# Kernel optimization log

Measured on AMD Instinct MI355X. Metric: run time of the kernel, lower is better.

Reference implementation:

```python
import jax, jax.numpy as jnp
import numpy as np

B, P, T = 64, 196, 30
E, D, A, ENC, V = 512, 512, 512, 512, 30000


def setup_inputs() -> dict:
    key = jax.random.key(0)
    ks = jax.random.split(key, 24)
    s = 0.02
    return {
        "encoder_feats": jax.random.normal(ks[0], (B, P, ENC), jnp.float32),
        "encoder_pooled": jax.random.normal(ks[1], (B, ENC), jnp.float32),
        "captions": jax.random.randint(ks[2], (B, T), 0, V),
        "We_att": jax.random.normal(ks[3], (ENC, A), jnp.float32) * s,
        "be_att": jnp.zeros((A,), jnp.float32),
        "Wd_att": jax.random.normal(ks[4], (D, A), jnp.float32) * s,
        "bd_att": jnp.zeros((A,), jnp.float32),
        "wf_att": jax.random.normal(ks[5], (A, 1), jnp.float32) * s,
        "bf_att": jnp.zeros((), jnp.float32),
        "emb_table": jax.random.normal(ks[6], (V, E), jnp.float32) * s,
        "W_ih": jax.random.normal(ks[7], (E + ENC, 4 * D), jnp.float32) * s,
        "W_hh": jax.random.normal(ks[8], (D, 4 * D), jnp.float32) * s,
        "b_ih": jnp.zeros((4 * D,), jnp.float32),
        "b_hh": jnp.zeros((4 * D,), jnp.float32),
        "W_init_h": jax.random.normal(ks[9], (ENC, D), jnp.float32) * s,
        "b_init_h": jnp.zeros((D,), jnp.float32),
        "W_init_c": jax.random.normal(ks[10], (ENC, D), jnp.float32) * s,
        "b_init_c": jnp.zeros((D,), jnp.float32),
        "W_fc": jax.random.normal(ks[11], (D, V), jnp.float32) * s,
        "b_fc": jnp.zeros((V,), jnp.float32),
        "W_beta": jax.random.normal(ks[12], (D, ENC), jnp.float32) * s,
        "b_beta": jnp.zeros((ENC,), jnp.float32),
    }


def reference(encoder_feats, encoder_pooled, captions, We_att, be_att, Wd_att,
              bd_att, wf_att, bf_att, emb_table, W_ih, W_hh, b_ih, b_hh,
              W_init_h, b_init_h, W_init_c, b_init_c, W_fc, b_fc, W_beta, b_beta):
    # teacher_forcing_ratio = 1.0, dropout in eval mode (identity)
    emb = emb_table[captions]                              # (B, T, E)
    h = jnp.tanh(encoder_pooled @ W_init_h + b_init_h)     # (B, D)
    c = jnp.tanh(encoder_pooled @ W_init_c + b_init_c)
    enc_proj = encoder_feats @ We_att + be_att             # (B, P, A) precomputed

    def step(carry, emb_t):
        h, c = carry
        dec_proj = h @ Wd_att + bd_att                     # (B, A)
        e = jnp.tanh(enc_proj + dec_proj[:, None, :])      # (B, P, A)
        scores = jnp.squeeze(e @ wf_att, -1) + bf_att      # (B, P)
        alpha = jax.nn.softmax(scores, axis=1)
        ctx = jnp.einsum('bp,bpd->bd', alpha, encoder_feats)
        gate = jax.nn.sigmoid(h @ W_beta + b_beta)
        ctx = gate * ctx
        x = jnp.concatenate([emb_t, ctx], axis=1)          # (B, E+ENC)
        gates = x @ W_ih + b_ih + h @ W_hh + b_hh          # (B, 4D) torch order i,f,g,o
        i, f, g, o = jnp.split(gates, 4, axis=1)
        c2 = jax.nn.sigmoid(f) * c + jax.nn.sigmoid(i) * jnp.tanh(g)
        h2 = jax.nn.sigmoid(o) * jnp.tanh(c2)
        out = h2 @ W_fc + b_fc                             # (B, V)
        return (h2, c2), out

    # inputs at steps t=1..T-1 are teacher-forced embeddings[:, t-1]
    xs = jnp.swapaxes(emb[:, :-1, :], 0, 1)                # (T-1, B, E)
    _, outs = jax.lax.scan(step, (h, c), xs)               # (T-1, B, V)
    outs = jnp.swapaxes(outs, 0, 1)                        # (B, T-1, V)
    zero0 = jnp.zeros((outs.shape[0], 1, outs.shape[2]), outs.dtype)
    return jnp.concatenate([zero0, outs], axis=1)          # (B, T, V)
```

## Files before the change

kernel.cpp:

```cpp
#include <hip/hip_runtime.h>
#include <hip/hip_bf16.h>

#define BB 64
#define PP 196
#define TT 30
#define DD 512
#define VV 30000
#define VPAD 30080
#define MROWS 1856
#define MPAD 1920
#define NBLK 64
#define ASTR 3072
#define ABUF ((size_t)64 * ASTR)

typedef __attribute__((ext_vector_type(8))) short short8;
typedef __attribute__((ext_vector_type(4))) float f32x4;

__device__ __forceinline__ unsigned short f2bf(float f) {
    unsigned int u = __float_as_uint(f);
    unsigned int r = u + 0x7FFFu + ((u >> 16) & 1u);
    return (unsigned short)(r >> 16);
}
__device__ __forceinline__ float bf2f(unsigned short u) {
    return __uint_as_float(((unsigned int)u) << 16);
}
__device__ __forceinline__ float sigf(float x) { return 1.f / (1.f + __expf(-x)); }
__device__ __forceinline__ float tanh_fast(float x) { return 1.f - 2.f / (1.f + __expf(2.f * x)); }
__device__ __forceinline__ unsigned int pack2(unsigned short a, unsigned short b) {
    return (unsigned int)a | ((unsigned int)b << 16);
}
__device__ __forceinline__ void ast_u32(unsigned int* p, unsigned int v) {
    __hip_atomic_store(p, v, __ATOMIC_RELAXED, __HIP_MEMORY_SCOPE_AGENT);
}
__device__ __forceinline__ void ast_f32(float* p, float v) {
    __hip_atomic_store(p, v, __ATOMIC_RELAXED, __HIP_MEMORY_SCOPE_AGENT);
}

__global__ __launch_bounds__(256) void k_cast(const float* __restrict__ in,
                                              unsigned short* __restrict__ out, int n) {
    int i = blockIdx.x * 256 + threadIdx.x;
    int stride = gridDim.x * 256;
    for (; i < n; i += stride) out[i] = f2bf(in[i]);
}

__global__ __launch_bounds__(256) void k_transpose_cast(const float* __restrict__ in,
                                                        unsigned short* __restrict__ out,
                                                        int R, int C, int Cpad, int ostride, int ooff) {
    __shared__ float tile[32][33];
    int tx = threadIdx.x & 31, ty = threadIdx.x >> 5;
    int c0 = blockIdx.x * 32, r0 = blockIdx.y * 32;
#pragma unroll
    for (int i = 0; i < 4; ++i) {
        int r = r0 + ty + i * 8, c = c0 + tx;
        tile[ty + i * 8][tx] = (c < C) ? in[(size_t)r * C + c] : 0.f;
    }
    __syncthreads();
#pragma unroll
    for (int i = 0; i < 4; ++i) {
        int outr = c0 + ty + i * 8, outc = r0 + tx;
        if (outr < Cpad) out[(size_t)outr * ostride + ooff + outc] = f2bf(tile[tx][ty + i * 8]);
    }
}

__global__ __launch_bounds__(256) void k_transpose_cast_split(const float* __restrict__ in,
                                                              unsigned short* __restrict__ out,
                                                              int R, int C, int ostride,
                                                              int ooff, int looff) {
    __shared__ float tile[32][33];
    int tx = threadIdx.x & 31, ty = threadIdx.x >> 5;
    int c0 = blockIdx.x * 32, r0 = blockIdx.y * 32;
#pragma unroll
    for (int i = 0; i < 4; ++i) {
        int r = r0 + ty + i * 8, c = c0 + tx;
        tile[ty + i * 8][tx] = in[(size_t)r * C + c];
    }
    __syncthreads();
#pragma unroll
    for (int i = 0; i < 4; ++i) {
        int outr = c0 + ty + i * 8, outc = r0 + tx;
        float v = tile[tx][ty + i * 8];
        unsigned short hi = f2bf(v);
        unsigned short lo = f2bf(v - bf2f(hi));
        out[(size_t)outr * ostride + ooff + outc] = hi;
        out[(size_t)outr * ostride + looff + outc] = lo;
    }
}

__global__ __launch_bounds__(256) void k_zero0(float* __restrict__ out) {
    int i = blockIdx.x * 256 + threadIdx.x;
    int b = i / VV, v = i - b * VV;
    out[(size_t)b * (TT * VV) + v] = 0.f;
}

__global__ __launch_bounds__(256) void k_init(const float* __restrict__ pooled,
                                              const float* __restrict__ Wh, const float* __restrict__ bh,
                                              const float* __restrict__ Wc, const float* __restrict__ bc,
                                              unsigned short* __restrict__ A1,
                                              float* __restrict__ cbuf, int* __restrict__ bar) {
    int b = blockIdx.x >> 1, which = blockIdx.x & 1, t = threadIdx.x;
    if (blockIdx.x == 0) {
        for (int i = t; i < NBLK * 32 + 32; i += 256) bar[i] = 0;
    }
    const float* W = which ? Wc : Wh;
    const float* bias = which ? bc : bh;
    const float* pr = pooled + b * DD;
    float a0 = 0.f, a1 = 0.f;
#pragma unroll 4
    for (int k = 0; k < DD; ++k) {
        float pv = pr[k];
        a0 += pv * W[k * DD + t];
        a1 += pv * W[k * DD + t + 256];
    }
    float v0 = tanh_fast(a0 + bias[t]);
    float v1 = tanh_fast(a1 + bias[t + 256]);
    if (which == 0) {
        unsigned short hi0 = f2bf(v0), lo0 = f2bf(v0 - bf2f(hi0));
        unsigned short hi1 = f2bf(v1), lo1 = f2bf(v1 - bf2f(hi1));
        unsigned short* xr = A1 + b * ASTR;
        xr[1024 + t] = hi0;        xr[2560 + t] = lo0;
        xr[1024 + t + 256] = hi1;  xr[2560 + t + 256] = lo1;
    } else {
        cbuf[b * DD + t] = v0;
        cbuf[b * DD + t + 256] = v1;
    }
}

__device__ __forceinline__ void gbar(int* bar, int g) {
    __syncthreads();
    asm volatile("s_waitcnt vmcnt(0)" ::: "memory");
    if (blockIdx.x == 0) {
        int t = threadIdx.x;
        if (t >= 1 && t < NBLK) {
            while (__hip_atomic_load(&bar[t * 32], __ATOMIC_RELAXED, __HIP_MEMORY_SCOPE_AGENT) < g)
                __builtin_amdgcn_s_sleep(1);
        }
        __syncthreads();
        if (t == 0)
            __hip_atomic_store(&bar[NBLK * 32], g, __ATOMIC_RELAXED, __HIP_MEMORY_SCOPE_AGENT);
    } else {
        if (threadIdx.x == 0) {
            __hip_atomic_store(&bar[blockIdx.x * 32], g, __ATOMIC_RELAXED, __HIP_MEMORY_SCOPE_AGENT);
            while (__hip_atomic_load(&bar[NBLK * 32], __ATOMIC_RELAXED, __HIP_MEMORY_SCOPE_AGENT) < g)
                __builtin_amdgcn_s_sleep(1);
        }
        __syncthreads();
    }
}

__global__ __launch_bounds__(256, 1) void k_recur(
    const unsigned short* __restrict__ ep,
    const unsigned short* __restrict__ fb,
    const unsigned short* __restrict__ WdbT,
    const unsigned short* __restrict__ WT,
    const float* __restrict__ bd,
    const float* __restrict__ bbeta,
    const float* __restrict__ wfv,
    const int* __restrict__ caps,
    const float* __restrict__ emb,
    const float* __restrict__ b_ih,
    const float* __restrict__ b_hh,
    unsigned short* __restrict__ A_rot,
    float* __restrict__ cbuf,
    float* __restrict__ dpb_rot,
    unsigned short* __restrict__ hb,
    int* __restrict__ bar) {

    const int blk = blockIdx.x, t = threadIdx.x;
    const int lane = t & 63, wave = t >> 6;
    const int r16 = lane & 15, kg = lane >> 4;
    const int swz = kg ^ ((r16 >> 1) & 3);

    __shared__ unsigned short Bp_s[16 * 1024];
    __shared__ unsigned short Sa[2][2048];
    __shared__ unsigned short Sl[2][2048];
    __shared__ unsigned short Sb[2][2048];
    __shared__ unsigned short Sbl[2][2048];
    __shared__ float sc_s[256];
    __shared__ float red_s[16];
    __shared__ float ctx_s[4][512];

    const int srow = t >> 2, scs = t & 3;
    const int scsrc = scs ^ ((srow >> 1) & 3);

    {
        const unsigned short* src = WdbT + (size_t)(blk * 16) * 1024;
#pragma unroll
        for (int cc = 0; cc < 8; ++cc) {
            int c = t + cc * 256;
            int row = c >> 7, u = c & 127;
            ((uint4*)Bp_s)[row * 128 + (u ^ (row & 7))] =
                *(const uint4*)(src + (size_t)row * 1024 + u * 8);
        }
    }
    __syncthreads();

    int gph = 0;

    for (int ts = 1; ts < TT; ++ts) {
        unsigned short* Acur = A_rot + (size_t)ts * ABUF;
        unsigned short* Anext = Acur + ABUF;
        float* dpb = dpb_rot + (size_t)(ts - 1) * 64 * 1024;

        {
            const int n0 = blk * 16;
            const unsigned short* Ah = Acur + srow * ASTR + 1024 + scsrc * 8;
            const unsigned short* Al = Acur + srow * ASTR + 2560 + scsrc * 8;
            f32x4 acc = {0.f, 0.f, 0.f, 0.f};
            uint4 p0h = *(const uint4*)(Ah + 0), p0l = *(const uint4*)(Al + 0);
            uint4 p1h = *(const uint4*)(Ah + 32), p1l = *(const uint4*)(Al + 32);
#pragma unroll 1
            for (int i = 0; i < 16; i += 2) {
                ((uint4*)Sa[0])[t] = p0h;
                ((uint4*)Sl[0])[t] = p0l;
                { int kn = (i + 2 < 16 ? i + 2 : i) * 32;
                  p0h = *(const uint4*)(Ah + kn); p0l = *(const uint4*)(Al + kn); }
                __syncthreads();
                {
                    int k0 = i * 32;
                    short8 ah = *(const short8*)&Sa[0][((wave * 16 + r16) * 4 + swz) * 8];
                    short8 al = *(const short8*)&Sl[0][((wave * 16 + r16) * 4 + swz) * 8];
                    int cu = (k0 >> 3) + kg;
                    short8 bh = *(const short8*)&Bp_s[r16 * 1024 + ((cu ^ (r16 & 7)) << 3)];
                    short8 bl = *(const short8*)&Bp_s[r16 * 1024 + (((cu + 64) ^ (r16 & 7)) << 3)];
                    acc = __builtin_amdgcn_mfma_f32_16x16x32_bf16(ah, bh, acc, 0, 0, 0);
                    acc = __builtin_amdgcn_mfma_f32_16x16x32_bf16(al, bh, acc, 0, 0, 0);
                    acc = __builtin_amdgcn_mfma_f32_16x16x32_bf16(ah, bl, acc, 0, 0, 0);
                }
                ((uint4*)Sa[1])[t] = p1h;
                ((uint4*)Sl[1])[t] = p1l;
                { int kn = (i + 3 < 16 ? i + 3 : i + 1) * 32;
                  p1h = *(const uint4*)(Ah + kn); p1l = *(const uint4*)(Al + kn); }
                __syncthreads();
                {
                    int k0 = (i + 1) * 32;
                    short8 ah = *(const short8*)&Sa[1][((wave * 16 + r16) * 4 + swz) * 8];
                    short8 al = *(const short8*)&Sl[1][((wave * 16 + r16) * 4 + swz) * 8];
                    int cu = (k0 >> 3) + kg;
                    short8 bh = *(const short8*)&Bp_s[r16 * 1024 + ((cu ^ (r16 & 7)) << 3)];
                    short8 bl = *(const short8*)&Bp_s[r16 * 1024 + (((cu + 64) ^ (r16 & 7)) << 3)];
                    acc = __builtin_amdgcn_mfma_f32_16x16x32_bf16(ah, bh, acc, 0, 0, 0);
                    acc = __builtin_amdgcn_mfma_f32_16x16x32_bf16(al, bh, acc, 0, 0, 0);
                    acc = __builtin_amdgcn_mfma_f32_16x16x32_bf16(ah, bl, acc, 0, 0, 0);
                }
            }
            int col = n0 + r16;
#pragma unroll
            for (int r = 0; r < 4; ++r) {
                int b = wave * 16 + kg * 4 + r;
                float v = acc[r];
                if (col < 512) ast_f32(&dpb[b * 1024 + col], v + bd[col]);
                else ast_f32(&dpb[b * 1024 + col], sigf(v + bbeta[col - 512]));
            }
        }
        gbar(bar, ++gph);

        {
            const int b = blk;
            const int d8 = lane * 8;
            float dsl[8], wsl[8];
            {
                float4 dv0 = *(const float4*)(dpb + b * 1024 + d8);
                float4 dv1 = *(const float4*)(dpb + b * 1024 + d8 + 4);
                float4 wv0 = *(const float4*)(wfv + d8);
                float4 wv1 = *(const float4*)(wfv + d8 + 4);
                dsl[0] = dv0.x; dsl[1] = dv0.y; dsl[2] = dv0.z; dsl[3] = dv0.w;
                dsl[4] = dv1.x; dsl[5] = dv1.y; dsl[6] = dv1.z; dsl[7] = dv1.w;
                wsl[0] = wv0.x; wsl[1] = wv0.y; wsl[2] = wv0.z; wsl[3] = wv0.w;
                wsl[4] = wv1.x; wsl[5] = wv1.y; wsl[6] = wv1.z; wsl[7] = wv1.w;
            }
            const unsigned short* epb = ep + (size_t)(b * PP) * 512;
#pragma unroll 1
            for (int bb = 0; bb < 6; ++bb) {
                uint4 pk[8];
#pragma unroll
                for (int u = 0; u < 8; ++u)
                    pk[u] = *(const uint4*)(epb + (size_t)(wave + 4 * (bb * 8 + u)) * 512 + d8);
#pragma unroll
                for (int u = 0; u < 8; ++u) {
                    const unsigned short* pu = (const unsigned short*)&pk[u];
                    float s = 0.f;
#pragma unroll
                    for (int j = 0; j < 8; ++j)
                        s += tanh_fast(bf2f(pu[j]) + dsl[j]) * wsl[j];
#pragma unroll
                    for (int off = 32; off; off >>= 1) s += __shfl_xor(s, off);
                    if (lane == 0) sc_s[wave + 4 * (bb * 8 + u)] = s;
                }
            }
            {
                uint4 pk = *(const uint4*)(epb + (size_t)(wave + 192) * 512 + d8);
                const unsigned short* pu = (const unsigned short*)&pk;
                float s = 0.f;
#pragma unroll
                for (int j = 0; j < 8; ++j)
                    s += tanh_fast(bf2f(pu[j]) + dsl[j]) * wsl[j];
#pragma unroll
                for (int off = 32; off; off >>= 1) s += __shfl_xor(s, off);
                if (lane == 0) sc_s[wave + 192] = s;
            }
            __syncthreads();
            float sv = (t < PP) ? sc_s[t] : -1e30f;
            float m = sv;
#pragma unroll
            for (int off = 32; off; off >>= 1) m = fmaxf(m, __shfl_xor(m, off));
            if (lane == 0) red_s[wave] = m;
            __syncthreads();
            float mx = fmaxf(fmaxf(red_s[0], red_s[1]), fmaxf(red_s[2], red_s[3]));
            float e = (t < PP) ? __expf(sv - mx) : 0.f;
            float ssum = e;
#pragma unroll
            for (int off = 32; off; off >>= 1) ssum += __shfl_xor(ssum, off);
            if (lane == 0) red_s[8 + wave] = ssum;
            __syncthreads();
            float inv = 1.f / (red_s[8] + red_s[9] + red_s[10] + red_s[11]);
            if (t < PP) sc_s[t] = e * inv;
            __syncthreads();
            const unsigned short* fbb = fb + (size_t)(b * PP) * 512;
            float c[8];
#pragma unroll
            for (int j = 0; j < 8; ++j) c[j] = 0.f;
#pragma unroll 1
            for (int bb = 0; bb < 6; ++bb) {
                uint4 pk[8];
                float av[8];
#pragma unroll
                for (int u = 0; u < 8; ++u) {
                    int p = wave + 4 * (bb * 8 + u);
                    pk[u] = *(const uint4*)(fbb + (size_t)p * 512 + d8);
                    av[u] = sc_s[p];
                }
#pragma unroll
                for (int u = 0; u < 8; ++u) {
                    const unsigned short* pu = (const unsigned short*)&pk[u];
#pragma unroll
                    for (int j = 0; j < 8; ++j) c[j] += av[u] * bf2f(pu[j]);
                }
            }
            {
                int p = wave + 192;
                uint4 pk = *(const uint4*)(fbb + (size_t)p * 512 + d8);
                float a = sc_s[p];
                const unsigned short* pu = (const unsigned short*)&pk;
#pragma unroll
                for (int j = 0; j < 8; ++j) c[j] += a * bf2f(pu[j]);
            }
#pragma unroll
            for (int j = 0; j < 8; ++j) ctx_s[wave][d8 + j] = c[j];
            __syncthreads();
            float2 c0v = *(const float2*)&ctx_s[0][2 * t];
            float2 c1v = *(const float2*)&ctx_s[1][2 * t];
            float2 c2v = *(const float2*)&ctx_s[2][2 * t];
            float2 c3v = *(const float2*)&ctx_s[3][2 * t];
            float ctx0 = c0v.x + c1v.x + c2v.x + c3v.x;
            float ctx1 = c0v.y + c1v.y + c2v.y + c3v.y;
            float2 bt2 = *(const float2*)(dpb + b * 1024 + 512 + 2 * t);
            int tok = caps[b * TT + (ts - 1)];
            const float* er = emb + (size_t)tok * 512;
            float2 ev = *(const float2*)(er + 2 * t);
            unsigned int* xr32 = (unsigned int*)(Acur + (size_t)b * ASTR);
            unsigned short e0h = f2bf(ev.x), e1h = f2bf(ev.y);
            ast_u32(xr32 + t, pack2(e0h, e1h));
            ast_u32(xr32 + 768 + t, pack2(f2bf(ev.x - bf2f(e0h)), f2bf(ev.y - bf2f(e1h))));
            float g0 = bt2.x * ctx0, g1 = bt2.y * ctx1;
            unsigned short g0h = f2bf(g0), g1h = f2bf(g1);
            ast_u32(xr32 + 256 + t, pack2(g0h, g1h));
            ast_u32(xr32 + 1024 + t, pack2(f2bf(g0 - bf2f(g0h)), f2bf(g1 - bf2f(g1h))));
        }
        gbar(bar, ++gph);

        if (blk < 32) {
            const int d0 = blk * 16;
            const unsigned short* Ah = Acur + srow * ASTR + scsrc * 8;
            const unsigned short* Al = Ah + 1536;
            const int jrow = ((srow >> 4) << 9) + d0 + (srow & 15);
            const unsigned short* Bh = WT + (size_t)jrow * 3072 + scsrc * 8;
            const unsigned short* Bl = Bh + 1536;
            f32x4 acc[4];
#pragma unroll
            for (int g = 0; g < 4; ++g) acc[g] = {0.f, 0.f, 0.f, 0.f};
            uint4 a0h = *(const uint4*)(Ah + 0), a0l = *(const uint4*)(Al + 0);
            uint4 b0h = *(const uint4*)(Bh + 0), b0l = *(const uint4*)(Bl + 0);
            uint4 a1h = *(const uint4*)(Ah + 32), a1l = *(const uint4*)(Al + 32);
            uint4 b1h = *(const uint4*)(Bh + 32), b1l = *(const uint4*)(Bl + 32);
#pragma unroll 1
            for (int i = 0; i < 48; i += 2) {
                ((uint4*)Sa[0])[t] = a0h; ((uint4*)Sl[0])[t] = a0l;
                ((uint4*)Sb[0])[t] = b0h; ((uint4*)Sbl[0])[t] = b0l;
                { int kn = (i + 2 < 48 ? i + 2 : i) * 32;
                  a0h = *(const uint4*)(Ah + kn); a0l = *(const uint4*)(Al + kn);
                  b0h = *(const uint4*)(Bh + kn); b0l = *(const uint4*)(Bl + kn); }
                __syncthreads();
                {
                    short8 ah = *(const short8*)&Sa[0][((wave * 16 + r16) * 4 + swz) * 8];
                    short8 al = *(const short8*)&Sl[0][((wave * 16 + r16) * 4 + swz) * 8];
#pragma unroll
                    for (int g = 0; g < 4; ++g) {
                        short8 bh = *(const short8*)&Sb[0][((g * 16 + r16) * 4 + swz) * 8];
                        short8 bl = *(const short8*)&Sbl[0][((g * 16 + r16) * 4 + swz) * 8];
                        acc[g] = __builtin_amdgcn_mfma_f32_16x16x32_bf16(ah, bh, acc[g], 0, 0, 0);
                        acc[g] = __builtin_amdgcn_mfma_f32_16x16x32_bf16(al, bh, acc[g], 0, 0, 0);
                        acc[g] = __builtin_amdgcn_mfma_f32_16x16x32_bf16(ah, bl, acc[g], 0, 0, 0);
                    }
                }
                ((uint4*)Sa[1])[t] = a1h; ((uint4*)Sl[1])[t] = a1l;
                ((uint4*)Sb[1])[t] = b1h; ((uint4*)Sbl[1])[t] = b1l;
                { int kn = (i + 3 < 48 ? i + 3 : i + 1) * 32;
                  a1h = *(const uint4*)(Ah + kn); a1l = *(const uint4*)(Al + kn);
                  b1h = *(const uint4*)(Bh + kn); b1l = *(const uint4*)(Bl + kn); }
                __syncthreads();
                {
                    short8 ah = *(const short8*)&Sa[1][((wave * 16 + r16) * 4 + swz) * 8];
                    short8 al = *(const short8*)&Sl[1][((wave * 16 + r16) * 4 + swz) * 8];
#pragma unroll
                    for (int g = 0; g < 4; ++g) {
                        short8 bh = *(const short8*)&Sb[1][((g * 16 + r16) * 4 + swz) * 8];
                        short8 bl = *(const short8*)&Sbl[1][((g * 16 + r16) * 4 + swz) * 8];
                        acc[g] = __builtin_amdgcn_mfma_f32_16x16x32_bf16(ah, bh, acc[g], 0, 0, 0);
                        acc[g] = __builtin_amdgcn_mfma_f32_16x16x32_bf16(al, bh, acc[g], 0, 0, 0);
                        acc[g] = __builtin_amdgcn_mfma_f32_16x16x32_bf16(ah, bl, acc[g], 0, 0, 0);
                    }
                }
            }
            int d = d0 + r16;
            float bi_ = b_ih[d] + b_hh[d];
            float bf_ = b_ih[d + 512] + b_hh[d + 512];
            float bg_ = b_ih[d + 1024] + b_hh[d + 1024];
            float bo_ = b_ih[d + 1536] + b_hh[d + 1536];
#pragma unroll
            for (int r = 0; r < 4; ++r) {
                int b = wave * 16 + kg * 4 + r;
                float gi = sigf(acc[0][r] + bi_);
                float gf = sigf(acc[1][r] + bf_);
                float gg = tanh_fast(acc[2][r] + bg_);
                float go = sigf(acc[3][r] + bo_);
                float cn = gf * cbuf[b * 512 + d] + gi * gg;
                float hn = go * tanh_fast(cn);
                cbuf[b * 512 + d] = cn;
                unsigned short hhi = f2bf(hn);
                unsigned short hlo = f2bf(hn - bf2f(hhi));
                hb[(size_t)((ts - 1) * 64 + b) * 512 + d] = hhi;
                int oh = __shfl_xor((int)hhi, 1);
                int ol = __shfl_xor((int)hlo, 1);
                if ((r16 & 1) == 0) {
                    unsigned int* rw = (unsigned int*)(Anext + (size_t)b * ASTR);
                    ast_u32(rw + 512 + (d >> 1), pack2(hhi, (unsigned short)oh));
                    ast_u32(rw + 1280 + (d >> 1), pack2(hlo, (unsigned short)ol));
                }
            }
        }
        gbar(bar, ++gph);
    }
}

template <int MODE>
__global__ __launch_bounds__(256) void gemm_mfma(const unsigned short* __restrict__ A,
                                                 const unsigned short* __restrict__ Bt,
                                                 const float* __restrict__ bias,
                                                 void* __restrict__ Cv) {
    constexpr int K = 512;
    __shared__ unsigned short As[128 * 32];
    __shared__ unsigned short Bs[128 * 32];
    const int t = threadIdx.x;
    const int m0 = blockIdx.y * 128;
    const int n0 = blockIdx.x * 128;
    const int lane = t & 63, wave = t >> 6;
    const int wm = wave >> 1, wn = wave & 1;
    const int r16 = lane & 15, kg = lane >> 4;
    const int swz = kg ^ ((r16 >> 1) & 3);

    f32x4 acc[4][4];
#pragma unroll
    for (int i = 0; i < 4; ++i)
#pragma unroll
        for (int j = 0; j < 4; ++j) acc[i][j] = {0.f, 0.f, 0.f, 0.f};

    const short8* As8 = (const short8*)As;
    const short8* Bs8 = (const short8*)Bs;

    for (int k0 = 0; k0 < K; k0 += 32) {
#pragma unroll
        for (int i = 0; i < 2; ++i) {
            int u = t + i * 256;
            int row = u >> 2, cs = u & 3;
            int csrc = cs ^ ((row >> 1) & 3);
            ((uint4*)As)[u] = *(const uint4*)(A + (size_t)(m0 + row) * K + k0 + csrc * 8);
            ((uint4*)Bs)[u] = *(const uint4*)(Bt + (size_t)(n0 + row) * K + k0 + csrc * 8);
        }
        __syncthreads();
        short8 af[4], bfr[4];
#pragma unroll
        for (int i = 0; i < 4; ++i) af[i] = As8[(wm * 64 + i * 16 + r16) * 4 + swz];
#pragma unroll
        for (int j = 0; j < 4; ++j) bfr[j] = Bs8[(wn * 64 + j * 16 + r16) * 4 + swz];
#pragma unroll
        for (int i = 0; i < 4; ++i)
#pragma unroll
            for (int j = 0; j < 4; ++j)
                acc[i][j] = __builtin_amdgcn_mfma_f32_16x16x32_bf16(af[i], bfr[j], acc[i][j], 0, 0, 0);
        __syncthreads();
    }

#pragma unroll
    for (int i = 0; i < 4; ++i) {
#pragma unroll
        for (int j = 0; j < 4; ++j) {
            int colg = n0 + wn * 64 + j * 16 + r16;
            float bv;
            if (MODE == 0) bv = bias[colg];
            else bv = (colg < VV) ? bias[colg] : 0.f;
#pragma unroll
            for (int r = 0; r < 4; ++r) {
                int rowg = m0 + wm * 64 + i * 16 + kg * 4 + r;
                float v = acc[i][j][r] + bv;
                if (MODE == 0) {
                    ((unsigned short*)Cv)[(size_t)rowg * 512 + colg] = f2bf(v);
                } else {
                    if (rowg < MROWS && colg < VV) {
                        int tt = rowg >> 6, bb2 = rowg & 63;
                        ((float*)Cv)[(size_t)bb2 * (TT * VV) + (size_t)(tt + 1) * VV + colg] = v;
                    }
                }
            }
        }
    }
}

extern "C" void kernel_launch(void* const* d_in, const int* in_sizes, int n_in,
                              void* d_out, int out_size, void* d_ws, size_t ws_size,
                              hipStream_t stream) {
    const float* feats   = (const float*)d_in[0];
    const float* pooled  = (const float*)d_in[1];
    const int*   caps    = (const int*)d_in[2];
    const float* We      = (const float*)d_in[3];
    const float* be      = (const float*)d_in[4];
    const float* Wd      = (const float*)d_in[5];
    const float* bd      = (const float*)d_in[6];
    const float* wfv     = (const float*)d_in[7];
    const float* emb     = (const float*)d_in[9];
    const float* W_ih    = (const float*)d_in[10];
    const float* W_hh    = (const float*)d_in[11];
    const float* b_ih    = (const float*)d_in[12];
    const float* b_hh    = (const float*)d_in[13];
    const float* W_inh   = (const float*)d_in[14];
    const float* b_inh   = (const float*)d_in[15];
    const float* W_inc   = (const float*)d_in[16];
    const float* b_inc   = (const float*)d_in[17];
    const float* Wfc     = (const float*)d_in[18];
    const float* bfc     = (const float*)d_in[19];
    const float* Wbeta   = (const float*)d_in[20];
    const float* bbeta   = (const float*)d_in[21];
    float* out = (float*)d_out;

    char* ws = (char*)d_ws;
    size_t off = 0;
    auto alloc = [&](size_t bytes) -> char* {
        char* p = ws + off;
        off += (bytes + 255) & ~(size_t)255;
        return p;
    };
    unsigned short* ep_bf = (unsigned short*)alloc((size_t)12544 * 512 * 2);
    unsigned short* fb    = (unsigned short*)alloc((size_t)12544 * 512 * 2);
    unsigned short* WeT   = (unsigned short*)alloc((size_t)512 * 512 * 2);
    unsigned short* WfcT  = (unsigned short*)alloc((size_t)VPAD * 512 * 2);
    unsigned short* WdbT  = (unsigned short*)alloc((size_t)1024 * 1024 * 2);
    unsigned short* WT    = (unsigned short*)alloc((size_t)2048 * 3072 * 2);
    unsigned short* hb    = (unsigned short*)alloc((size_t)MPAD * 512 * 2);
    unsigned short* A_rot = (unsigned short*)alloc((size_t)31 * ABUF * 2);
    float*          dpb   = (float*)alloc((size_t)30 * 64 * 1024 * 4);
    float*          cbuf  = (float*)alloc((size_t)64 * 512 * 4);
    int*            bar   = (int*)alloc((size_t)(NBLK * 32 + 32) * 4);
    (void)ws_size; (void)in_sizes; (void)n_in; (void)out_size;

    k_cast<<<2048, 256, 0, stream>>>(feats, fb, 12544 * 512);
    k_transpose_cast<<<dim3(16, 16), 256, 0, stream>>>(We, WeT, 512, 512, 512, 512, 0);
    k_transpose_cast<<<dim3(940, 16), 256, 0, stream>>>(Wfc, WfcT, 512, VV, VPAD, 512, 0);
    k_transpose_cast_split<<<dim3(16, 16), 256, 0, stream>>>(Wd, WdbT, 512, 512, 1024, 0, 512);
    k_transpose_cast_split<<<dim3(16, 16), 256, 0, stream>>>(Wbeta, WdbT + (size_t)512 * 1024, 512, 512, 1024, 0, 512);
    k_transpose_cast_split<<<dim3(64, 32), 256, 0, stream>>>(W_ih, WT, 1024, 2048, 3072, 0, 1536);
    k_transpose_cast_split<<<dim3(64, 16), 256, 0, stream>>>(W_hh, WT, 512, 2048, 3072, 1024, 2560);
    k_init<<<128, 256, 0, stream>>>(pooled, W_inh, b_inh, W_inc, b_inc, A_rot + ABUF, cbuf, bar);
    gemm_mfma<0><<<dim3(4, 98), 256, 0, stream>>>(fb, WeT, be, ep_bf);
    k_zero0<<<7500, 256, 0, stream>>>(out);

    k_recur<<<NBLK, 256, 0, stream>>>(ep_bf, fb, WdbT, WT, bd, bbeta, wfv, caps, emb,
                                      b_ih, b_hh, A_rot, cbuf, dpb, hb, bar);

    gemm_mfma<1><<<dim3(235, 15), 256, 0, stream>>>(hb, WfcT, bfc, out);
}
```

Before: 2.284 ms.

## Deepen global prefetch, use raw s_barrier, and flatten grid barrier

Both per-step MFMA loops in the recurrent kernel now keep four stages of global loads in flight in registers instead of two. They also replace __syncthreads with an LDS-only wait plus s_barrier, so outstanding global prefetches are not drained at every tile. The grid barrier changes from a master-gather/broadcast scheme to one where every block publishes its flag and polls all others directly, removing a hop of latency. The costs are higher register pressure and more polling traffic on the flag lines.

```diff
diff --git a/kernel.cpp b/kernel.cpp
--- a/kernel.cpp
+++ b/kernel.cpp
@@ -128,24 +128,53 @@
 __device__ __forceinline__ void gbar(int* bar, int g) {
     __syncthreads();
     asm volatile("s_waitcnt vmcnt(0)" ::: "memory");
-    if (blockIdx.x == 0) {
-        int t = threadIdx.x;
-        if (t >= 1 && t < NBLK) {
-            while (__hip_atomic_load(&bar[t * 32], __ATOMIC_RELAXED, __HIP_MEMORY_SCOPE_AGENT) < g)
-                __builtin_amdgcn_s_sleep(1);
-        }
-        __syncthreads();
-        if (t == 0)
-            __hip_atomic_store(&bar[NBLK * 32], g, __ATOMIC_RELAXED, __HIP_MEMORY_SCOPE_AGENT);
-    } else {
-        if (threadIdx.x == 0) {
-            __hip_atomic_store(&bar[blockIdx.x * 32], g, __ATOMIC_RELAXED, __HIP_MEMORY_SCOPE_AGENT);
-            while (__hip_atomic_load(&bar[NBLK * 32], __ATOMIC_RELAXED, __HIP_MEMORY_SCOPE_AGENT) < g)
-                __builtin_amdgcn_s_sleep(1);
-        }
-        __syncthreads();
-    }
-}
+    if (threadIdx.x == 0)
+        __hip_atomic_store(&bar[blockIdx.x * 32], g, __ATOMIC_RELAXED, __HIP_MEMORY_SCOPE_AGENT);
+    if (threadIdx.x < NBLK) {
+        while (__hip_atomic_load(&bar[threadIdx.x * 32], __ATOMIC_RELAXED, __HIP_MEMORY_SCOPE_AGENT) < g)
+            __builtin_amdgcn_s_sleep(1);
+    }
+    __syncthreads();
+}
+
+#define PA_SUB(S, PH, PL, TILE, NEXT)                                                          \
+    ((uint4*)Sa[S])[t] = PH;                                                                   \
+    ((uint4*)Sl[S])[t] = PL;                                                                   \
+    { int kn = (NEXT) * 32; PH = *(const uint4*)(Ah + kn); PL = *(const uint4*)(Al + kn); }    \
+    asm volatile("s_waitcnt lgkmcnt(0)" ::: "memory");                                         \
+    __builtin_amdgcn_sched_barrier(0);                                                         \
+    __builtin_amdgcn_s_barrier();                                                              \
+    __builtin_amdgcn_sched_barrier(0);                                                         \
+    { int k0 = (TILE) * 32;                                                                    \
+      short8 ah = *(const short8*)&Sa[S][((wave * 16 + r16) * 4 + swz) * 8];                   \
+      short8 al = *(const short8*)&Sl[S][((wave * 16 + r16) * 4 + swz) * 8];                   \
+      int cu = (k0 >> 3) + kg;                                                                 \
+      short8 bh = *(const short8*)&Bp_s[r16 * 1024 + ((cu ^ (r16 & 7)) << 3)];                 \
+      short8 bl = *(const short8*)&Bp_s[r16 * 1024 + (((cu + 64) ^ (r16 & 7)) << 3)];          \
+      acc = __builtin_amdgcn_mfma_f32_16x16x32_bf16(ah, bh, acc, 0, 0, 0);                     \
+      acc = __builtin_amdgcn_mfma_f32_16x16x32_bf16(al, bh, acc, 0, 0, 0);                     \
+      acc = __builtin_amdgcn_mfma_f32_16x16x32_bf16(ah, bl, acc, 0, 0, 0); }
+
+#define PC_SUB(S, RAH, RAL, RBH, RBL, TILE, NEXT)                                              \
+    ((uint4*)Sa[S])[t] = RAH;  ((uint4*)Sl[S])[t] = RAL;                                       \
+    ((uint4*)Sb[S])[t] = RBH;  ((uint4*)Sbl[S])[t] = RBL;                                      \
+    { int kn = (NEXT) * 32;                                                                    \
+      RAH = *(const uint4*)(Ah + kn); RAL = *(const uint4*)(Al + kn);                          \
+      RBH = *(const uint4*)(Bh + kn); RBL = *(const uint4*)(Bl + kn); }                        \
+    asm volatile("s_waitcnt lgkmcnt(0)" ::: "memory");                                         \
+    __builtin_amdgcn_sched_barrier(0);                                                         \
+    __builtin_amdgcn_s_barrier();                                                              \
+    __builtin_amdgcn_sched_barrier(0);                                                         \
+    { short8 ah = *(const short8*)&Sa[S][((wave * 16 + r16) * 4 + swz) * 8];                   \
+      short8 al = *(const short8*)&Sl[S][((wave * 16 + r16) * 4 + swz) * 8];                   \
+      _Pragma("unroll")                                                                        \
+      for (int g = 0; g < 4; ++g) {                                                            \
+          short8 bh = *(const short8*)&Sb[S][((g * 16 + r16) * 4 + swz) * 8];                  \
+          short8 bl = *(const short8*)&Sbl[S][((g * 16 + r16) * 4 + swz) * 8];                 \
+          acc[g] = __builtin_amdgcn_mfma_f32_16x16x32_bf16(ah, bh, acc[g], 0, 0, 0);           \
+          acc[g] = __builtin_amdgcn_mfma_f32_16x16x32_bf16(al, bh, acc[g], 0, 0, 0);           \
+          acc[g] = __builtin_amdgcn_mfma_f32_16x16x32_bf16(ah, bl, acc[g], 0, 0, 0);           \
+      } }
 
 __global__ __launch_bounds__(256, 1) void k_recur(
     const unsigned short* __restrict__ ep,
@@ -206,42 +235,16 @@
             const unsigned short* Ah = Acur + srow * ASTR + 1024 + scsrc * 8;
             const unsigned short* Al = Acur + srow * ASTR + 2560 + scsrc * 8;
             f32x4 acc = {0.f, 0.f, 0.f, 0.f};
-            uint4 p0h = *(const uint4*)(Ah + 0), p0l = *(const uint4*)(Al + 0);
+            uint4 p0h = *(const uint4*)(Ah + 0),  p0l = *(const uint4*)(Al + 0);
             uint4 p1h = *(const uint4*)(Ah + 32), p1l = *(const uint4*)(Al + 32);
+            uint4 p2h = *(const uint4*)(Ah + 64), p2l = *(const uint4*)(Al + 64);
+            uint4 p3h = *(const uint4*)(Ah + 96), p3l = *(const uint4*)(Al + 96);
 #pragma unroll 1
-            for (int i = 0; i < 16; i += 2) {
-                ((uint4*)Sa[0])[t] = p0h;
-                ((uint4*)Sl[0])[t] = p0l;
-                { int kn = (i + 2 < 16 ? i + 2 : i) * 32;
-                  p0h = *(const uint4*)(Ah + kn); p0l = *(const uint4*)(Al + kn); }
-                __syncthreads();
-                {
-                    int k0 = i * 32;
-                    short8 ah = *(const short8*)&Sa[0][((wave * 16 + r16) * 4 + swz) * 8];
-                    short8 al = *(const short8*)&Sl[0][((wave * 16 + r16) * 4 + swz) * 8];
-                    int cu = (k0 >> 3) + kg;
-                    short8 bh = *(const short8*)&Bp_s[r16 * 1024 + ((cu ^ (r16 & 7)) << 3)];
-                    short8 bl = *(const short8*)&Bp_s[r16 * 1024 + (((cu + 64) ^ (r16 & 7)) << 3)];
-                    acc = __builtin_amdgcn_mfma_f32_16x16x32_bf16(ah, bh, acc, 0, 0, 0);
-                    acc = __builtin_amdgcn_mfma_f32_16x16x32_bf16(al, bh, acc, 0, 0, 0);
-                    acc = __builtin_amdgcn_mfma_f32_16x16x32_bf16(ah, bl, acc, 0, 0, 0);
-                }
-                ((uint4*)Sa[1])[t] = p1h;
-                ((uint4*)Sl[1])[t] = p1l;
-                { int kn = (i + 3 < 16 ? i + 3 : i + 1) * 32;
-                  p1h = *(const uint4*)(Ah + kn); p1l = *(const uint4*)(Al + kn); }
-                __syncthreads();
-                {
-                    int k0 = (i + 1) * 32;
-                    short8 ah = *(const short8*)&Sa[1][((wave * 16 + r16) * 4 + swz) * 8];
-                    short8 al = *(const short8*)&Sl[1][((wave * 16 + r16) * 4 + swz) * 8];
-                    int cu = (k0 >> 3) + kg;
-                    short8 bh = *(const short8*)&Bp_s[r16 * 1024 + ((cu ^ (r16 & 7)) << 3)];
-                    short8 bl = *(const short8*)&Bp_s[r16 * 1024 + (((cu + 64) ^ (r16 & 7)) << 3)];
-                    acc = __builtin_amdgcn_mfma_f32_16x16x32_bf16(ah, bh, acc, 0, 0, 0);
-                    acc = __builtin_amdgcn_mfma_f32_16x16x32_bf16(al, bh, acc, 0, 0, 0);
-                    acc = __builtin_amdgcn_mfma_f32_16x16x32_bf16(ah, bl, acc, 0, 0, 0);
-                }
+            for (int i = 0; i < 16; i += 4) {
+                PA_SUB(0, p0h, p0l, i + 0, (i + 4 < 16 ? i + 4 : i + 0))
+                PA_SUB(1, p1h, p1l, i + 1, (i + 5 < 16 ? i + 5 : i + 1))
+                PA_SUB(0, p2h, p2l, i + 2, (i + 6 < 16 ? i + 6 : i + 2))
+                PA_SUB(1, p3h, p3l, i + 3, (i + 7 < 16 ? i + 7 : i + 3))
             }
             int col = n0 + r16;
 #pragma unroll
@@ -378,48 +381,20 @@
             f32x4 acc[4];
 #pragma unroll
             for (int g = 0; g < 4; ++g) acc[g] = {0.f, 0.f, 0.f, 0.f};
-            uint4 a0h = *(const uint4*)(Ah + 0), a0l = *(const uint4*)(Al + 0);
-            uint4 b0h = *(const uint4*)(Bh + 0), b0l = *(const uint4*)(Bl + 0);
+            uint4 a0h = *(const uint4*)(Ah + 0),  a0l = *(const uint4*)(Al + 0);
+            uint4 b0h = *(const uint4*)(Bh + 0),  b0l = *(const uint4*)(Bl + 0);
             uint4 a1h = *(const uint4*)(Ah + 32), a1l = *(const uint4*)(Al + 32);
             uint4 b1h = *(const uint4*)(Bh + 32), b1l = *(const uint4*)(Bl + 32);
+            uint4 a2h = *(const uint4*)(Ah + 64), a2l = *(const uint4*)(Al + 64);
+            uint4 b2h = *(const uint4*)(Bh + 64), b2l = *(const uint4*)(Bl + 64);
+            uint4 a3h = *(const uint4*)(Ah + 96), a3l = *(const uint4*)(Al + 96);
+            uint4 b3h = *(const uint4*)(Bh + 96), b3l = *(const uint4*)(Bl + 96);
 #pragma unroll 1
-            for (int i = 0; i < 48; i += 2) {
-                ((uint4*)Sa[0])[t] = a0h; ((uint4*)Sl[0])[t] = a0l;
-                ((uint4*)Sb[0])[t] = b0h; ((uint4*)Sbl[0])[t] = b0l;
-                { int kn = (i + 2 < 48 ? i + 2 : i) * 32;
-                  a0h = *(const uint4*)(Ah + kn); a0l = *(const uint4*)(Al + kn);
-                  b0h = *(const uint4*)(Bh + kn); b0l = *(const uint4*)(Bl + kn); }
-                __syncthreads();
-                {
-                    short8 ah = *(const short8*)&Sa[0][((wave * 16 + r16) * 4 + swz) * 8];
-                    short8 al = *(const short8*)&Sl[0][((wave * 16 + r16) * 4 + swz) * 8];
-#pragma unroll
-                    for (int g = 0; g < 4; ++g) {
-                        short8 bh = *(const short8*)&Sb[0][((g * 16 + r16) * 4 + swz) * 8];
-                        short8 bl = *(const short8*)&Sbl[0][((g * 16 + r16) * 4 + swz) * 8];
-                        acc[g] = __builtin_amdgcn_mfma_f32_16x16x32_bf16(ah, bh, acc[g], 0, 0, 0);
-                        acc[g] = __builtin_amdgcn_mfma_f32_16x16x32_bf16(al, bh, acc[g], 0, 0, 0);
-                        acc[g] = __builtin_amdgcn_mfma_f32_16x16x32_bf16(ah, bl, acc[g], 0, 0, 0);
-                    }
-                }
-                ((uint4*)Sa[1])[t] = a1h; ((uint4*)Sl[1])[t] = a1l;
-                ((uint4*)Sb[1])[t] = b1h; ((uint4*)Sbl[1])[t] = b1l;
-                { int kn = (i + 3 < 48 ? i + 3 : i + 1) * 32;
-                  a1h = *(const uint4*)(Ah + kn); a1l = *(const uint4*)(Al + kn);
-                  b1h = *(const uint4*)(Bh + kn); b1l = *(const uint4*)(Bl + kn); }
-                __syncthreads();
-                {
-                    short8 ah = *(const short8*)&Sa[1][((wave * 16 + r16) * 4 + swz) * 8];
-                    short8 al = *(const short8*)&Sl[1][((wave * 16 + r16) * 4 + swz) * 8];
-#pragma unroll
-                    for (int g = 0; g < 4; ++g) {
-                        short8 bh = *(const short8*)&Sb[1][((g * 16 + r16) * 4 + swz) * 8];
-                        short8 bl = *(const short8*)&Sbl[1][((g * 16 + r16) * 4 + swz) * 8];
-                        acc[g] = __builtin_amdgcn_mfma_f32_16x16x32_bf16(ah, bh, acc[g], 0, 0, 0);
-                        acc[g] = __builtin_amdgcn_mfma_f32_16x16x32_bf16(al, bh, acc[g], 0, 0, 0);
-                        acc[g] = __builtin_amdgcn_mfma_f32_16x16x32_bf16(ah, bl, acc[g], 0, 0, 0);
-                    }
-                }
+            for (int i = 0; i < 48; i += 4) {
+                PC_SUB(0, a0h, a0l, b0h, b0l, i + 0, (i + 4 < 48 ? i + 4 : i + 0))
+                PC_SUB(1, a1h, a1l, b1h, b1l, i + 1, (i + 5 < 48 ? i + 5 : i + 1))
+                PC_SUB(0, a2h, a2l, b2h, b2l, i + 2, (i + 6 < 48 ? i + 6 : i + 2))
+                PC_SUB(1, a3h, a3l, b3h, b3l, i + 3, (i + 7 < 48 ? i + 7 : i + 3))
             }
             int d = d0 + r16;
             float bi_ = b_ih[d] + b_hh[d];
```

After: 2.187 ms. 1.04x faster.
